# Performance work log

Hardware: AMD Instinct MI355X
Metric: run time of the kernel (lower is better)

## Reference

```python
import jax, jax.numpy as jnp
import numpy as np

N = 50000   # nodes
E = 800000  # edges (avg degree 16)
D = 128     # feature dim
H = 4       # heads
Dh = D // H # per-head dim = 32


def setup_inputs() -> dict:
    key = jax.random.key(0)
    ks = jax.random.split(key, 12)
    inp = {
        "x": jax.random.normal(ks[0], (N, D), jnp.float32),
        "edge_index": jax.random.randint(ks[1], (2, E), 0, N, dtype=jnp.int64),
    }
    i = 2
    for l in range(2):
        for nm in ("q", "k", "v", "s"):
            inp[f"{nm}_w{l}"] = jax.random.normal(ks[i], (D, D), jnp.float32) / np.float32(np.sqrt(D))
            inp[f"{nm}_b{l}"] = jnp.zeros((D,), jnp.float32)
        i += 1
    return inp


def _transformer_conv(x, src, dst, qw, qb, kw, kb, vw, vb, sw, sb):
    """PyG TransformerConv: concat heads, root_weight skip, softmax over in-edges."""
    n = x.shape[0]
    q = (x @ qw + qb).reshape(n, H, Dh)
    k = (x @ kw + kb).reshape(n, H, Dh)
    v = (x @ vw + vb).reshape(n, H, Dh)
    # per-edge attention logits [E, H]
    logits = jnp.einsum('ehd,ehd->eh', q[dst], k[src]) / jnp.sqrt(jnp.float32(Dh))
    # segment softmax over edges grouped by destination node
    m = jax.ops.segment_max(logits, dst, num_segments=n)          # [N, H]
    e = jnp.exp(logits - m[dst])                                  # [E, H]
    s = jax.ops.segment_sum(e, dst, num_segments=n)               # [N, H]
    alpha = e / (s[dst] + 1e-16)                                  # [E, H]
    msg = v[src] * alpha[:, :, None]                              # [E, H, Dh]
    out = jax.ops.segment_sum(msg, dst, num_segments=n)           # [N, H, Dh]
    out = out.reshape(n, H * Dh)
    return out + x @ sw + sb  # root skip (lin_skip)


def reference(x, edge_index,
              q_w0, q_b0, k_w0, k_b0, v_w0, v_b0, s_w0, s_b0,
              q_w1, q_b1, k_w1, k_b1, v_w1, v_b1, s_w1, s_b1):
    src, dst = edge_index[0], edge_index[1]
    h = _transformer_conv(x, src, dst, q_w0, q_b0, k_w0, k_b0, v_w0, v_b0, s_w0, s_b0)
    h = jax.nn.relu(h)  # dropout is identity in eval mode
    h = _transformer_conv(h, src, dst, q_w1, q_b1, k_w1, k_b1, v_w1, v_b1, s_w1, s_b1)
    return h
```

## Files before the change

### kernel.cpp

```cpp
#include <hip/hip_runtime.h>
#include <math.h>

#define NN 50000
#define NR 50016
#define EE 800000
#define SCALE 0.17677669529663687f
#define MAXDEG 64
#define NRANGE 4
#define RSPAN (NN / NRANGE)
#define NSLICE 250
#define ESLICE (EE / NSLICE)

typedef __attribute__((ext_vector_type(8))) short short8;
typedef __attribute__((ext_vector_type(4))) float floatx4;
typedef __attribute__((ext_vector_type(4))) int intx4;
typedef unsigned short ushort_t;

#if defined(__has_builtin)
#  if __has_builtin(__builtin_amdgcn_fdot2_f32_bf16)
#    define HAVE_BF16_DOT2 1
#  endif
#endif
#ifndef HAVE_BF16_DOT2
#  define HAVE_BF16_DOT2 0
#endif
#if HAVE_BF16_DOT2
typedef __attribute__((ext_vector_type(2))) __bf16 bf16x2;
#endif

static __device__ __forceinline__ float bf2f(ushort_t u) {
    union { unsigned int i; float f; } x; x.i = ((unsigned int)u) << 16; return x.f;
}
static __device__ __forceinline__ ushort_t f2bf(float f) {
    union { float fv; unsigned int i; } x; x.fv = f;
    unsigned int lsb = (x.i >> 16) & 1u;
    x.i += 0x7fffu + lsb;
    return (ushort_t)(x.i >> 16);
}

static __device__ __forceinline__ float dot8bf(short8 k8, short8 q8, float p) {
#if HAVE_BF16_DOT2
    union { short8 s; unsigned int u[4]; } ku, qu;
    ku.s = k8; qu.s = q8;
#pragma unroll
    for (int i = 0; i < 4; ++i) {
        union { unsigned int u; bf16x2 h; } a, b;
        a.u = ku.u[i]; b.u = qu.u[i];
        p = __builtin_amdgcn_fdot2_f32_bf16(a.h, b.h, p, false);
    }
#else
#pragma unroll
    for (int i = 0; i < 8; ++i)
        p += bf2f((ushort_t)k8[i]) * bf2f((ushort_t)q8[i]);
#endif
    return p;
}

__global__ void k_detect(const int* __restrict__ ei, int* __restrict__ flag) {
    int any = 0;
#pragma unroll
    for (int i = 0; i < 4; ++i) any |= ei[2 * (threadIdx.x * 4 + i) + 1];
    unsigned long long b = __ballot(any != 0);
    if (threadIdx.x == 0) *flag = (b == 0ull) ? 1 : 0;
}

static __device__ __forceinline__ int edge_src(const int* ei, int is64, int e) {
    return is64 ? ei[2 * e] : ei[e];
}
static __device__ __forceinline__ int edge_dst(const int* ei, int is64, int e) {
    return is64 ? ei[2 * (EE + e)] : ei[EE + e];
}

__global__ void k_prep_weights(const float* q0, const float* k0,
                               const float* v0, const float* s0,
                               const float* q1, const float* k1,
                               const float* v1, const float* s1,
                               ushort_t* wt0, ushort_t* wt1) {
    int widx = blockIdx.x >> 3;
    const float* src =
        (widx == 0) ? q0 : (widx == 1) ? k0 : (widx == 2) ? v0 : (widx == 3) ? s0 :
        (widx == 4) ? q1 : (widx == 5) ? k1 : (widx == 6) ? v1 : s1;
    ushort_t* dst = ((widx < 4) ? wt0 : wt1) + (size_t)(widx & 3) * (128 * 128);
    int it0 = (blockIdx.x & 7) * 8;
    for (int it = it0; it < it0 + 8; ++it) {
        int idx = it * 256 + threadIdx.x;
        int j    = idx & 7;
        int lane = (idx >> 3) & 63;
        int t    = (idx >> 9) & 7;
        int kkb  = idx >> 12;
        int kk = kkb * 32 + (lane >> 4) * 8 + j;
        int c  = t * 16 + (lane & 15);
        dst[idx] = f2bf(src[kk * 128 + c]);
    }
}

__global__ void k_compact(const int* __restrict__ ei, const int* __restrict__ flag,
                          int* __restrict__ pairs) {
    int e = blockIdx.x * blockDim.x + threadIdx.x;
    if (e < EE) {
        int is64 = *flag;
        pairs[2 * e]     = edge_dst(ei, is64, e);
        pairs[2 * e + 1] = edge_src(ei, is64, e);
    }
}

__global__ __launch_bounds__(256) void k_fillp(
    const int* __restrict__ pairs,
    int* __restrict__ cnt, int* __restrict__ col) {
    int range = blockIdx.x & (NRANGE - 1);
    int slice = blockIdx.x >> 2;
    int lo = range * RSPAN, hi = lo + RSPAN;
    const int* p = pairs + (size_t)slice * ESLICE * 2;
    for (int i = threadIdx.x; i < ESLICE / 2; i += 256) {
        intx4 v = *(const intx4*)(p + i * 4);
        int d0 = v[0], d1 = v[2];
        if (d0 >= lo && d0 < hi) {
            int pos = atomicAdd(&cnt[d0], 1);
            if (pos < MAXDEG) col[d0 * MAXDEG + pos] = v[1];
        }
        if (d1 >= lo && d1 < hi) {
            int pos = atomicAdd(&cnt[d1], 1);
            if (pos < MAXDEG) col[d1 * MAXDEG + pos] = v[3];
        }
    }
}

template <bool F32A>
__global__ __launch_bounds__(256) void k_gemm_qkvs(
    const void* __restrict__ Av,
    const ushort_t* __restrict__ Wp,
    const float* __restrict__ qb, const float* __restrict__ kb,
    const float* __restrict__ vb, const float* __restrict__ sb,
    ushort_t* __restrict__ Q, ushort_t* __restrict__ KV,
    ushort_t* __restrict__ S) {
    __shared__ ushort_t sA[32][136];
    int wave = threadIdx.x >> 6;
    int lane = threadIdx.x & 63;
    int quad = lane >> 4;
    int lm = lane & 15;
    int row0 = blockIdx.x * 32;

    if (F32A) {
        int r  = threadIdx.x >> 3;
        int c0 = (threadIdx.x & 7) * 16;
        int rr = row0 + r; if (rr > NN - 1) rr = NN - 1;
        const float* srcp = (const float*)Av + (size_t)rr * 128 + c0;
        floatx4 v0 = *(const floatx4*)(srcp);
        floatx4 v1 = *(const floatx4*)(srcp + 4);
        floatx4 v2 = *(const floatx4*)(srcp + 8);
        floatx4 v3 = *(const floatx4*)(srcp + 12);
        short8 o0, o1;
#pragma unroll
        for (int i = 0; i < 4; ++i) {
            o0[i]     = (short)f2bf(v0[i]); o0[i + 4] = (short)f2bf(v1[i]);
            o1[i]     = (short)f2bf(v2[i]); o1[i + 4] = (short)f2bf(v3[i]);
        }
        *(short8*)&sA[r][c0]     = o0;
        *(short8*)&sA[r][c0 + 8] = o1;
    } else {
        const ushort_t* A = (const ushort_t*)Av;
#pragma unroll
        for (int it = 0; it < 2; ++it) {
            int r = it * 16 + (threadIdx.x >> 4);
            int c = (threadIdx.x & 15) * 8;
            *(short8*)&sA[r][c] = *(const short8*)(A + (size_t)(row0 + r) * 128 + c);
        }
    }
    __syncthreads();

    const ushort_t* wp = Wp + (size_t)wave * 16384;
    floatx4 acc[2][8];
#pragma unroll
    for (int rt = 0; rt < 2; ++rt)
#pragma unroll
        for (int t = 0; t < 8; ++t) acc[rt][t] = (floatx4)0.0f;

#pragma unroll
    for (int kkb = 0; kkb < 4; ++kkb) {
        short8 a0 = *(const short8*)&sA[lm][kkb * 32 + quad * 8];
        short8 a1 = *(const short8*)&sA[16 + lm][kkb * 32 + quad * 8];
#pragma unroll
        for (int t = 0; t < 8; ++t) {
            short8 b = *(const short8*)(wp + (size_t)((kkb * 8 + t) * 64 + lane) * 8);
            acc[0][t] = __builtin_amdgcn_mfma_f32_16x16x32_bf16(a0, b, acc[0][t], 0, 0, 0);
            acc[1][t] = __builtin_amdgcn_mfma_f32_16x16x32_bf16(a1, b, acc[1][t], 0, 0, 0);
        }
    }

    const float* bias = (wave == 0) ? qb : (wave == 1) ? kb : (wave == 2) ? vb : sb;
    ushort_t* O     = (wave == 0) ? Q  : (wave == 3) ? S : KV;
    int       strd  = (wave == 1 || wave == 2) ? 256 : 128;
    int       cofs  = (wave == 2) ? 128 : 0;
#pragma unroll
    for (int rt = 0; rt < 2; ++rt)
#pragma unroll
        for (int t = 0; t < 8; ++t) {
            int c = t * 16 + lm;
            float bv = bias[c];
#pragma unroll
            for (int r = 0; r < 4; ++r) {
                int row = row0 + rt * 16 + quad * 4 + r;
                O[(size_t)row * strd + cofs + c] = f2bf(acc[rt][t][r] + bv);
            }
        }
}

__global__ __launch_bounds__(256) void k_attn(
    const ushort_t* __restrict__ Q, const ushort_t* __restrict__ KV,
    const ushort_t* __restrict__ S,
    const int* __restrict__ cnt, const int* __restrict__ col,
    ushort_t* __restrict__ outb, float* __restrict__ outf, int do_relu) {
    int wave = threadIdx.x >> 6;
    int lane = threadIdx.x & 63;
    int g = lane >> 3;
    int sub = lane & 7;
    int node = blockIdx.x * 4 + wave;
    if (node >= NN) return;

    const ushort_t* qrow = Q + (size_t)node * 128 + sub * 16;
    short8 qa = *(const short8*)qrow;
    short8 qb8 = *(const short8*)(qrow + 8);

    int deg = cnt[node]; if (deg > MAXDEG) deg = MAXDEG;
    const int* crow = col + node * MAXDEG;
    float l = 0.f;
    float acc[16];
#pragma unroll
    for (int i = 0; i < 16; ++i) acc[i] = 0.f;

    int e = g;
    int s = (e < deg) ? crow[e] : 0;
    while (e < deg) {
        const ushort_t* kv = KV + (size_t)s * 256 + sub * 16;
        short8 ka = *(const short8*)kv;
        short8 kb8 = *(const short8*)(kv + 8);
        short8 va = *(const short8*)(kv + 128);
        short8 vb8 = *(const short8*)(kv + 136);
        int e2 = e + 8;
        int s2 = (e2 < deg) ? crow[e2] : 0;
        float p = 0.f;
        p = dot8bf(ka, qa, p);
        p = dot8bf(kb8, qb8, p);
        p += __shfl_xor(p, 1);
        float w = __expf(p * SCALE);
        l += w;
#pragma unroll
        for (int i = 0; i < 8; ++i) {
            acc[i]     += w * bf2f((ushort_t)va[i]);
            acc[i + 8] += w * bf2f((ushort_t)vb8[i]);
        }
        e = e2; s = s2;
    }

#pragma unroll
    for (int off = 8; off <= 32; off <<= 1) {
        l += __shfl_xor(l, off);
#pragma unroll
        for (int i = 0; i < 16; ++i) acc[i] += __shfl_xor(acc[i], off);
    }

    if (g == 0) {
        float inv = 1.0f / (l + 1e-16f);
        const ushort_t* srow = S + (size_t)node * 128 + sub * 16;
        short8 sa = *(const short8*)srow;
        short8 sb8 = *(const short8*)(srow + 8);
        float o[16];
#pragma unroll
        for (int i = 0; i < 8; ++i) {
            o[i]     = acc[i]     * inv + bf2f((ushort_t)sa[i]);
            o[i + 8] = acc[i + 8] * inv + bf2f((ushort_t)sb8[i]);
        }
        if (do_relu)
#pragma unroll
            for (int i = 0; i < 16; ++i) o[i] = fmaxf(o[i], 0.f);
        if (outb) {
            short8 ob0, ob1;
#pragma unroll
            for (int i = 0; i < 8; ++i) {
                ob0[i] = (short)f2bf(o[i]);
                ob1[i] = (short)f2bf(o[i + 8]);
            }
            *(short8*)(outb + (size_t)node * 128 + sub * 16)     = ob0;
            *(short8*)(outb + (size_t)node * 128 + sub * 16 + 8) = ob1;
        }
        if (outf) {
#pragma unroll
            for (int t = 0; t < 4; ++t) {
                floatx4 ov;
#pragma unroll
                for (int i = 0; i < 4; ++i) ov[i] = o[t * 4 + i];
                *(floatx4*)(outf + (size_t)node * 128 + sub * 16 + t * 4) = ov;
            }
        }
    }
}

extern "C" void kernel_launch(void* const* d_in, const int* in_sizes, int n_in,
                              void* d_out, int out_size, void* d_ws, size_t ws_size,
                              hipStream_t stream) {
    const float* x  = (const float*)d_in[0];
    const int*   ei = (const int*)d_in[1];
    const float* qw0 = (const float*)d_in[2];
    const float* qb0 = (const float*)d_in[3];
    const float* kw0 = (const float*)d_in[4];
    const float* kb0 = (const float*)d_in[5];
    const float* vw0 = (const float*)d_in[6];
    const float* vb0 = (const float*)d_in[7];
    const float* sw0 = (const float*)d_in[8];
    const float* sb0 = (const float*)d_in[9];
    const float* qw1 = (const float*)d_in[10];
    const float* qb1 = (const float*)d_in[11];
    const float* kw1 = (const float*)d_in[12];
    const float* kb1 = (const float*)d_in[13];
    const float* vw1 = (const float*)d_in[14];
    const float* vb1 = (const float*)d_in[15];
    const float* sw1 = (const float*)d_in[16];
    const float* sb1 = (const float*)d_in[17];

    char* ws = (char*)d_ws;
    size_t off = 0;
    auto alloc = [&](size_t bytes) -> void* {
        void* p = ws + off;
        off = (off + bytes + 255) & ~(size_t)255;
        return p;
    };
    int* flag       = (int*)alloc(4);
    int* cnt        = (int*)alloc((size_t)NN * 4);
    int* pairs      = (int*)alloc((size_t)EE * 8);
    int* colp       = (int*)alloc((size_t)NN * MAXDEG * 4);
    ushort_t* wt0   = (ushort_t*)alloc((size_t)512 * 128 * 2);
    ushort_t* wt1   = (ushort_t*)alloc((size_t)512 * 128 * 2);
    ushort_t* Q     = (ushort_t*)alloc((size_t)NR * 128 * 2);
    ushort_t* KV    = (ushort_t*)alloc((size_t)NR * 256 * 2);
    ushort_t* S     = (ushort_t*)alloc((size_t)NR * 128 * 2);
    ushort_t* h1b   = (ushort_t*)alloc((size_t)NR * 128 * 2);
    (void)ws_size; (void)in_sizes; (void)n_in; (void)out_size;

    (void)hipMemsetAsync(cnt, 0, (size_t)NN * 4, stream);
    k_detect<<<1, 64, 0, stream>>>(ei, flag);
    k_prep_weights<<<64, 256, 0, stream>>>(qw0, kw0, vw0, sw0, qw1, kw1, vw1, sw1, wt0, wt1);
    k_compact<<<(EE + 255) / 256, 256, 0, stream>>>(ei, flag, pairs);
    k_fillp<<<NSLICE * NRANGE, 256, 0, stream>>>(pairs, cnt, colp);

    k_gemm_qkvs<true><<<NR / 32, 256, 0, stream>>>(x, wt0, qb0, kb0, vb0, sb0, Q, KV, S);
    k_attn<<<(NN + 3) / 4, 256, 0, stream>>>(Q, KV, S, cnt, colp, h1b, nullptr, 1);

    k_gemm_qkvs<false><<<NR / 32, 256, 0, stream>>>(h1b, wt1, qb1, kb1, vb1, sb1, Q, KV, S);
    k_attn<<<(NN + 3) / 4, 256, 0, stream>>>(Q, KV, S, cnt, colp, nullptr,
                                             (float*)d_out, 0);
}
```

Before: 309.9 us.

## Map one 8-lane group per node in attention with software-prefetched edge loop

The attention kernel previously used a full wave per node, splitting edges across 8 lane groups and then reducing with cross-lane shuffles. Now each 8-lane group owns one node and walks all of its edges serially, prefetching the next neighbor's K/V row while computing on the current one. This removes the shuffle reduction and the idle lanes on low-degree nodes, and puts 32 nodes in each block. In exchange, per-node latency grows with degree, and warp divergence between nodes of different degree inside a wave may add imbalance.

Result: slower. 335.9 us (+8.4%).

```diff
diff --git a/kernel.cpp b/kernel.cpp
--- a/kernel.cpp
+++ b/kernel.cpp
@@ -210,87 +210,85 @@
     const ushort_t* __restrict__ S,
     const int* __restrict__ cnt, const int* __restrict__ col,
     ushort_t* __restrict__ outb, float* __restrict__ outf, int do_relu) {
-    int wave = threadIdx.x >> 6;
-    int lane = threadIdx.x & 63;
-    int g = lane >> 3;
-    int sub = lane & 7;
-    int node = blockIdx.x * 4 + wave;
+    int grp = threadIdx.x >> 3;
+    int sub = threadIdx.x & 7;
+    int node = blockIdx.x * 32 + grp;
     if (node >= NN) return;
 
     const ushort_t* qrow = Q + (size_t)node * 128 + sub * 16;
-    short8 qa = *(const short8*)qrow;
+    short8 qa  = *(const short8*)qrow;
     short8 qb8 = *(const short8*)(qrow + 8);
+    const ushort_t* srow = S + (size_t)node * 128 + sub * 16;
+    short8 sa  = *(const short8*)srow;
+    short8 sb8 = *(const short8*)(srow + 8);
 
     int deg = cnt[node]; if (deg > MAXDEG) deg = MAXDEG;
     const int* crow = col + node * MAXDEG;
+
     float l = 0.f;
     float acc[16];
 #pragma unroll
     for (int i = 0; i < 16; ++i) acc[i] = 0.f;
 
-    int e = g;
-    int s = (e < deg) ? crow[e] : 0;
-    while (e < deg) {
+    if (deg > 0) {
+        int s = crow[0];
         const ushort_t* kv = KV + (size_t)s * 256 + sub * 16;
-        short8 ka = *(const short8*)kv;
+        short8 ka  = *(const short8*)kv;
         short8 kb8 = *(const short8*)(kv + 8);
-        short8 va = *(const short8*)(kv + 128);
+        short8 va  = *(const short8*)(kv + 128);
         short8 vb8 = *(const short8*)(kv + 136);
-        int e2 = e + 8;
-        int s2 = (e2 < deg) ? crow[e2] : 0;
-        float p = 0.f;
-        p = dot8bf(ka, qa, p);
-        p = dot8bf(kb8, qb8, p);
-        p += __shfl_xor(p, 1);
-        float w = __expf(p * SCALE);
-        l += w;
+#pragma unroll 2
+        for (int e = 0; e < deg; ++e) {
+            int en = (e + 1 < deg) ? (e + 1) : e;
+            int s2 = crow[en];
+            const ushort_t* kv2 = KV + (size_t)s2 * 256 + sub * 16;
+            short8 nka  = *(const short8*)kv2;
+            short8 nkb  = *(const short8*)(kv2 + 8);
+            short8 nva  = *(const short8*)(kv2 + 128);
+            short8 nvb  = *(const short8*)(kv2 + 136);
+
+            float p = 0.f;
+            p = dot8bf(ka, qa, p);
+            p = dot8bf(kb8, qb8, p);
+            p += __shfl_xor(p, 1);
+            float w = __expf(p * SCALE);
+            l += w;
+#pragma unroll
+            for (int i = 0; i < 8; ++i) {
+                acc[i]     += w * bf2f((ushort_t)va[i]);
+                acc[i + 8] += w * bf2f((ushort_t)vb8[i]);
+            }
+            ka = nka; kb8 = nkb; va = nva; vb8 = nvb;
+        }
+    }
+
+    float inv = 1.0f / (l + 1e-16f);
+    float o[16];
+#pragma unroll
+    for (int i = 0; i < 8; ++i) {
+        o[i]     = acc[i]     * inv + bf2f((ushort_t)sa[i]);
+        o[i + 8] = acc[i + 8] * inv + bf2f((ushort_t)sb8[i]);
+    }
+    if (do_relu)
+#pragma unroll
+        for (int i = 0; i < 16; ++i) o[i] = fmaxf(o[i], 0.f);
+    if (outb) {
+        short8 ob0, ob1;
 #pragma unroll
         for (int i = 0; i < 8; ++i) {
-            acc[i]     += w * bf2f((ushort_t)va[i]);
-            acc[i + 8] += w * bf2f((ushort_t)vb8[i]);
-        }
-        e = e2; s = s2;
-    }
-
-#pragma unroll
-    for (int off = 8; off <= 32; off <<= 1) {
-        l += __shfl_xor(l, off);
-#pragma unroll
-        for (int i = 0; i < 16; ++i) acc[i] += __shfl_xor(acc[i], off);
-    }
-
-    if (g == 0) {
-        float inv = 1.0f / (l + 1e-16f);
-        const ushort_t* srow = S + (size_t)node * 128 + sub * 16;
-        short8 sa = *(const short8*)srow;
-        short8 sb8 = *(const short8*)(srow + 8);
-        float o[16];
-#pragma unroll
-        for (int i = 0; i < 8; ++i) {
-            o[i]     = acc[i]     * inv + bf2f((ushort_t)sa[i]);
-            o[i + 8] = acc[i + 8] * inv + bf2f((ushort_t)sb8[i]);
-        }
-        if (do_relu)
-#pragma unroll
-            for (int i = 0; i < 16; ++i) o[i] = fmaxf(o[i], 0.f);
-        if (outb) {
-            short8 ob0, ob1;
-#pragma unroll
-            for (int i = 0; i < 8; ++i) {
-                ob0[i] = (short)f2bf(o[i]);
-                ob1[i] = (short)f2bf(o[i + 8]);
-            }
-            *(short8*)(outb + (size_t)node * 128 + sub * 16)     = ob0;
-            *(short8*)(outb + (size_t)node * 128 + sub * 16 + 8) = ob1;
-        }
-        if (outf) {
-#pragma unroll
-            for (int t = 0; t < 4; ++t) {
-                floatx4 ov;
-#pragma unroll
-                for (int i = 0; i < 4; ++i) ov[i] = o[t * 4 + i];
-                *(floatx4*)(outf + (size_t)node * 128 + sub * 16 + t * 4) = ov;
-            }
+            ob0[i] = (short)f2bf(o[i]);
+            ob1[i] = (short)f2bf(o[i + 8]);
+        }
+        *(short8*)(outb + (size_t)node * 128 + sub * 16)     = ob0;
+        *(short8*)(outb + (size_t)node * 128 + sub * 16 + 8) = ob1;
+    }
+    if (outf) {
+#pragma unroll
+        for (int t = 0; t < 4; ++t) {
+            floatx4 ov;
+#pragma unroll
+            for (int i = 0; i < 4; ++i) ov[i] = o[t * 4 + i];
+            *(floatx4*)(outf + (size_t)node * 128 + sub * 16 + t * 4) = ov;
         }
     }
 }
@@ -343,9 +341,9 @@
     k_fillp<<<NSLICE * NRANGE, 256, 0, stream>>>(pairs, cnt, colp);
 
     k_gemm_qkvs<true><<<NR / 32, 256, 0, stream>>>(x, wt0, qb0, kb0, vb0, sb0, Q, KV, S);
-    k_attn<<<(NN + 3) / 4, 256, 0, stream>>>(Q, KV, S, cnt, colp, h1b, nullptr, 1);
+    k_attn<<<(NN + 31) / 32, 256, 0, stream>>>(Q, KV, S, cnt, colp, h1b, nullptr, 1);
 
     k_gemm_qkvs<false><<<NR / 32, 256, 0, stream>>>(h1b, wt1, qb1, kb1, vb1, sb1, Q, KV, S);
-    k_attn<<<(NN + 3) / 4, 256, 0, stream>>>(Q, KV, S, cnt, colp, nullptr,
-                                             (float*)d_out, 0);
-}
+    k_attn<<<(NN + 31) / 32, 256, 0, stream>>>(Q, KV, S, cnt, colp, nullptr,
+                                               (float*)d_out, 0);
+}
```
